# Kernel optimization log

Hardware: AMD Instinct MI355X
Metric: run time of the kernel (lower is better)

Reference implementation:

```python
import jax, jax.numpy as jnp
import numpy as np

NEG_SLOPE = 0.2  # PyG GATConv default leaky_relu slope
N_NODES, IN_DIM, HID, HEADS, OUT = 50000, 128, 64, 4, 128
N_EDGES = 800000


def gat_conv(x, src, dst, num_nodes, W, a_src, a_dst, bias, concat):
    """One PyG-style GATConv (add_self_loops already applied to src/dst)."""
    H, C = a_src.shape
    xp = (x @ W).reshape(num_nodes, H, C)            # (N,H,C)
    s = jnp.einsum('nhc,hc->nh', xp, a_src)          # per-node src score
    d = jnp.einsum('nhc,hc->nh', xp, a_dst)          # per-node dst score
    e = s[src] + d[dst]                              # (E,H)
    e = jnp.where(e > 0, e, NEG_SLOPE * e)           # leaky_relu
    # segment softmax over edges grouped by destination node
    m = jax.ops.segment_max(e, dst, num_segments=num_nodes)
    p = jnp.exp(e - m[dst])
    z = jax.ops.segment_sum(p, dst, num_segments=num_nodes)
    alpha = p / (z[dst] + 1e-16)                     # (E,H)
    # scatter-aggregate messages
    out = jax.ops.segment_sum(xp[src] * alpha[:, :, None], dst, num_segments=num_nodes)
    out = out.reshape(num_nodes, H * C) if concat else out.mean(axis=1)
    return out + bias


def setup_inputs() -> dict:
    key = jax.random.key(0)
    ks = jax.random.split(key, 16)
    HC = HEADS * HID
    inp = {
        'x': jax.random.normal(ks[0], (N_NODES, IN_DIM), dtype=jnp.float32),
        'edge_index': jax.random.randint(ks[1], (2, N_EDGES), 0, N_NODES, dtype=jnp.int32),
        'W0': jax.random.normal(ks[2], (IN_DIM, HC), dtype=jnp.float32) * 0.08,
        'a_src0': jax.random.normal(ks[3], (HEADS, HID), dtype=jnp.float32) * 0.1,
        'a_dst0': jax.random.normal(ks[4], (HEADS, HID), dtype=jnp.float32) * 0.1,
        'b0': jnp.zeros((HC,), dtype=jnp.float32),
        'W1': jax.random.normal(ks[5], (HC, HC), dtype=jnp.float32) * 0.06,
        'a_src1': jax.random.normal(ks[6], (HEADS, HID), dtype=jnp.float32) * 0.1,
        'a_dst1': jax.random.normal(ks[7], (HEADS, HID), dtype=jnp.float32) * 0.1,
        'b1': jnp.zeros((HC,), dtype=jnp.float32),
        'W2': jax.random.normal(ks[8], (HC, OUT), dtype=jnp.float32) * 0.06,
        'a_src2': jax.random.normal(ks[9], (1, OUT), dtype=jnp.float32) * 0.1,
        'a_dst2': jax.random.normal(ks[10], (1, OUT), dtype=jnp.float32) * 0.1,
        'b2': jnp.zeros((OUT,), dtype=jnp.float32),
    }
    return inp


def reference(x, edge_index, W0, a_src0, a_dst0, b0, W1, a_src1, a_dst1, b1, W2, a_src2, a_dst2, b2):
    N = x.shape[0]
    loops = jnp.arange(N, dtype=edge_index.dtype)  # add_self_loops=True
    src = jnp.concatenate([edge_index[0], loops])
    dst = jnp.concatenate([edge_index[1], loops])
    h = gat_conv(x, src, dst, N, W0, a_src0, a_dst0, b0, True)
    h = jax.nn.elu(h)
    h = gat_conv(h, src, dst, N, W1, a_src1, a_dst1, b1, True)
    h = jax.nn.elu(h)
    h = gat_conv(h, src, dst, N, W2, a_src2, a_dst2, b2, False)
    return h
```

## Files before the change

kernel.cpp:

```cpp
#include <hip/hip_runtime.h>
#include <hip/hip_bf16.h>
#include <hip/hip_fp16.h>
#include <math.h>

#define N_NODES 50000
#define N_EDGES 800000
#define ET      (N_EDGES + N_NODES)
#define IN_DIM  128
#define HEADS   4
#define HID     64
#define HC      256
#define OUTD    128

typedef _Float16 half8 __attribute__((ext_vector_type(8)));
typedef float f32x4 __attribute__((ext_vector_type(4)));


__global__ void hist_k(const int* __restrict__ ei, int* __restrict__ counts) {
    int i = blockIdx.x * blockDim.x + threadIdx.x;
    if (i >= ET) return;
    int dv = (i < N_EDGES) ? ei[N_EDGES + i] : (i - N_EDGES);
    atomicAdd(&counts[dv], 1);
}

__global__ void scan1_k(const int* __restrict__ counts, int* __restrict__ offs,
                        int* __restrict__ bsums) {
    __shared__ int sm[512];
    int tid = threadIdx.x;
    int i = blockIdx.x * 512 + tid;
    int v = (i < N_NODES) ? counts[i] : 0;
    sm[tid] = v;
    __syncthreads();
    #pragma unroll
    for (int o = 1; o < 512; o <<= 1) {
        int add = (tid >= o) ? sm[tid - o] : 0;
        __syncthreads();
        sm[tid] += add;
        __syncthreads();
    }
    if (i < N_NODES) offs[i] = sm[tid] - v;
    if (tid == 511) bsums[blockIdx.x] = sm[511];
}

__global__ void scan2_k(int* __restrict__ bsums, int nb) {
    __shared__ int sm[128];
    int tid = threadIdx.x;
    int v = (tid < nb) ? bsums[tid] : 0;
    sm[tid] = v;
    __syncthreads();
    #pragma unroll
    for (int o = 1; o < 128; o <<= 1) {
        int add = (tid >= o) ? sm[tid - o] : 0;
        __syncthreads();
        sm[tid] += add;
        __syncthreads();
    }
    if (tid < nb) bsums[tid] = sm[tid] - v;
}

__global__ void scan3_k(int* __restrict__ offs, const int* __restrict__ bsums) {
    int i = blockIdx.x * 512 + threadIdx.x;
    if (i < N_NODES) offs[i] += bsums[blockIdx.x];
    if (i == 0) offs[N_NODES] = ET;
}

__global__ void fill_k(const int* __restrict__ ei, const int* __restrict__ offs,
                       int* __restrict__ counts, int* __restrict__ csr) {
    int i = blockIdx.x * blockDim.x + threadIdx.x;
    if (i >= ET) return;
    int sv, dv;
    if (i < N_EDGES) { sv = ei[i]; dv = ei[N_EDGES + i]; }
    else             { sv = dv = i - N_EDGES; }
    int pos = offs[dv] + atomicSub(&counts[dv], 1) - 1;
    csr[pos] = sv;
}


__global__ void cvt_fp16_k(const float* __restrict__ x, __half* __restrict__ xh, int n4) {
    int i = blockIdx.x * 256 + threadIdx.x;
    if (i >= n4) return;
    float4 v = *(const float4*)(x + (size_t)i * 4);
    union { __half2 h2[2]; float2 f2; } u;
    u.h2[0] = __floats2half2_rn(v.x, v.y);
    u.h2[1] = __floats2half2_rn(v.z, v.w);
    *(float2*)(xh + (size_t)i * 4) = u.f2;
}

__global__ void prep_k(const float* __restrict__ W0, __half* __restrict__ Wt0,
                       const float* __restrict__ W1, __half* __restrict__ Wt1,
                       const float* __restrict__ W2, __half* __restrict__ Wt2,
                       float* __restrict__ S2, float* __restrict__ D2) {
    int idx = blockIdx.x * 256 + threadIdx.x;
    if (idx < 32768) {
        int n = idx / IN_DIM, k = idx - n * IN_DIM;
        Wt0[idx] = __float2half(W0[(size_t)k * HC + n]);
    } else if (idx < 98304) {
        int i = idx - 32768;
        int n = i / HC, k = i - n * HC;
        Wt1[i] = __float2half(W1[(size_t)k * HC + n]);
    } else if (idx < 131072) {
        int i = idx - 98304;
        int n = i / HC, k = i - n * HC;
        Wt2[i] = __float2half(W2[(size_t)k * OUTD + n]);
    } else if (idx < 181072) {
        S2[idx - 131072] = 0.f;
    } else if (idx < 231072) {
        D2[idx - 181072] = 0.f;
    }
}


__device__ __forceinline__ void async_copy16(void* lds_base, const void* gaddr) {
    __builtin_amdgcn_global_load_lds(
        (const __attribute__((address_space(1))) unsigned int*)gaddr,
        (__attribute__((address_space(3))) unsigned int*)lds_base,
        16, 0, 0);
}

template<int H, int CD, bool ATOMIC>
__global__ __launch_bounds__(256) void gemm_mfma_k(const __half* __restrict__ A,
                                                   const __half* __restrict__ Wt,
                                                   __half* __restrict__ C,
                                                   const float* __restrict__ asrc,
                                                   const float* __restrict__ adst,
                                                   float* __restrict__ S,
                                                   float* __restrict__ D,
                                                   int M, int K, int N) {
    __shared__ __attribute__((aligned(16))) __half Ah[128 * 64];
    __shared__ __attribute__((aligned(16))) __half Bh[128 * 64];
    const int t = threadIdx.x;
    const int w = t >> 6;
    const int lane = t & 63;
    const int wm = w >> 1, wn = w & 1;
    const int row0 = blockIdx.x * 128;
    const int col0 = blockIdx.y * 128;

    f32x4 acc[4][4];
    #pragma unroll
    for (int i = 0; i < 4; ++i)
        #pragma unroll
        for (int j = 0; j < 4; ++j) acc[i][j] = (f32x4){0.f, 0.f, 0.f, 0.f};

    const int srow = lane >> 3;
    const int skq  = (lane & 7) * 8;
    const int fr = lane & 15;
    const int fq = (lane >> 4) * 8;

    for (int k0 = 0; k0 < K; k0 += 64) {
        __syncthreads();
        #pragma unroll
        for (int hh = 0; hh < 4; ++hh) {
            int ra = row0 + w * 32 + hh * 8 + srow;
            if (ra > M - 1) ra = M - 1;
            async_copy16(&Ah[(w * 32 + hh * 8) * 64],
                         A + (size_t)ra * K + k0 + skq);
            int rb = col0 + w * 32 + hh * 8 + srow;
            async_copy16(&Bh[(w * 32 + hh * 8) * 64],
                         Wt + (size_t)rb * K + k0 + skq);
        }
        __syncthreads();
        #pragma unroll
        for (int c = 0; c < 2; ++c) {
            half8 a[4], b[4];
            #pragma unroll
            for (int i = 0; i < 4; ++i)
                a[i] = *(const half8*)&Ah[(wm * 64 + i * 16 + fr) * 64 + c * 32 + fq];
            #pragma unroll
            for (int j = 0; j < 4; ++j)
                b[j] = *(const half8*)&Bh[(wn * 64 + j * 16 + fr) * 64 + c * 32 + fq];
            #pragma unroll
            for (int i = 0; i < 4; ++i)
                #pragma unroll
                for (int j = 0; j < 4; ++j)
                    acc[i][j] = __builtin_amdgcn_mfma_f32_16x16x32_f16(a[i], b[j], acc[i][j], 0, 0, 0);
        }
    }

    const int cr = (lane >> 4) * 4;
    const int cc = lane & 15;
    #pragma unroll
    for (int i = 0; i < 4; ++i) {
        #pragma unroll
        for (int j = 0; j < 4; ++j) {
            int c = col0 + wn * 64 + j * 16 + cc;
            #pragma unroll
            for (int reg = 0; reg < 4; ++reg) {
                int r = row0 + wm * 64 + i * 16 + cr + reg;
                if (r < M)
                    C[(size_t)r * N + c] = __float2half(acc[i][j][reg]);
            }
        }
    }

    const int hh_ = ATOMIC ? 0 : (blockIdx.y * 2 + wn);
    float asj[4], adj[4];
    #pragma unroll
    for (int j = 0; j < 4; ++j) {
        int cwh = (ATOMIC ? wn * 64 : 0) + j * 16 + cc;
        asj[j] = asrc[hh_ * CD + cwh];
        adj[j] = adst[hh_ * CD + cwh];
    }
    #pragma unroll
    for (int i = 0; i < 4; ++i) {
        #pragma unroll
        for (int reg = 0; reg < 4; ++reg) {
            float sv = 0.f, dv = 0.f;
            #pragma unroll
            for (int j = 0; j < 4; ++j) {
                sv = fmaf(acc[i][j][reg], asj[j], sv);
                dv = fmaf(acc[i][j][reg], adj[j], dv);
            }
            #pragma unroll
            for (int o = 1; o < 16; o <<= 1) {
                sv += __shfl_xor(sv, o, 64);
                dv += __shfl_xor(dv, o, 64);
            }
            int r = row0 + wm * 64 + i * 16 + cr + reg;
            if (cc == 0 && r < M) {
                if constexpr (ATOMIC) {
                    atomicAdd(&S[r], sv);
                    atomicAdd(&D[r], dv);
                } else {
                    S[(size_t)r * H + hh_] = sv;
                    D[(size_t)r * H + hh_] = dv;
                }
            }
        }
    }
}


template<int H, int C, bool ELU_OUT, typename OT>
__global__ __launch_bounds__(256) void aggr_k(const __half* __restrict__ xp,
                                              const float* __restrict__ s,
                                              const float* __restrict__ d,
                                              const int* __restrict__ offs,
                                              const int* __restrict__ csr,
                                              const float* __restrict__ bias,
                                              OT* __restrict__ out) {
    constexpr int HCl = H * C;
    constexpr int EPL = HCl / 64;
    constexpr int U = 8;
    int wid = blockIdx.x * 4 + (threadIdx.x >> 6);
    int lane = threadIdx.x & 63;
    if (wid >= N_NODES) return;
    int h = (lane * EPL) / C;
    float dh = d[(size_t)wid * H + h];
    float z = 0.f;
    float acc[EPL];
    #pragma unroll
    for (int k = 0; k < EPL; ++k) acc[k] = 0.f;

    auto loadrow = [&](int src, float* v) {
        const __half* xr = xp + (size_t)src * HCl + lane * EPL;
        if constexpr (EPL == 4) {
            union { float2 f2; __half2 h2[2]; } u;
            u.f2 = *(const float2*)xr;
            float2 a = __half22float2(u.h2[0]);
            float2 b = __half22float2(u.h2[1]);
            v[0] = a.x; v[1] = a.y; v[2] = b.x; v[3] = b.y;
        } else {
            union { float f; __half2 h2; } u;
            u.f = *(const float*)xr;
            float2 a = __half22float2(u.h2);
            v[0] = a.x; v[1] = a.y;
        }
    };

    int e0 = offs[wid], e1 = offs[wid + 1];
    int j = e0;
    for (; j + U <= e1; j += U) {
        int srcs[U];
        #pragma unroll
        for (int u = 0; u < U; ++u) srcs[u] = csr[j + u];
        float ev[U];
        #pragma unroll
        for (int u = 0; u < U; ++u) ev[u] = s[(size_t)srcs[u] * H + h];
        float v[U][EPL];
        #pragma unroll
        for (int u = 0; u < U; ++u) loadrow(srcs[u], v[u]);
        #pragma unroll
        for (int u = 0; u < U; ++u) {
            float e = ev[u] + dh;
            e = (e > 0.f) ? e : 0.2f * e;
            float p = __expf(e);
            z += p;
            #pragma unroll
            for (int k = 0; k < EPL; ++k) acc[k] += p * v[u][k];
        }
    }
    for (; j < e1; ++j) {
        int sv = csr[j];
        float e = s[(size_t)sv * H + h] + dh;
        e = (e > 0.f) ? e : 0.2f * e;
        float p = __expf(e);
        float v[EPL];
        loadrow(sv, v);
        z += p;
        #pragma unroll
        for (int k = 0; k < EPL; ++k) acc[k] += p * v[k];
    }

    float inv = 1.f / (z + 1e-16f);
    float o[EPL];
    #pragma unroll
    for (int k = 0; k < EPL; ++k) {
        o[k] = acc[k] * inv + bias[lane * EPL + k];
        if constexpr (ELU_OUT) o[k] = (o[k] > 0.f) ? o[k] : (__expf(o[k]) - 1.f);
    }
    if constexpr (sizeof(OT) == 2 && EPL == 4) {
        union { __half2 h2[2]; float2 f2; } u;
        u.h2[0] = __floats2half2_rn(o[0], o[1]);
        u.h2[1] = __floats2half2_rn(o[2], o[3]);
        *(float2*)((__half*)out + (size_t)wid * HCl + lane * EPL) = u.f2;
    } else {
        #pragma unroll
        for (int k = 0; k < EPL; ++k)
            out[(size_t)wid * HCl + lane * EPL + k] = (OT)o[k];
    }
}


extern "C" void kernel_launch(void* const* d_in, const int* in_sizes, int n_in,
                              void* d_out, int out_size, void* d_ws, size_t ws_size,
                              hipStream_t stream) {
    const float* x      = (const float*)d_in[0];
    const int*   ei     = (const int*)  d_in[1];
    const float* W0     = (const float*)d_in[2];
    const float* as0    = (const float*)d_in[3];
    const float* ad0    = (const float*)d_in[4];
    const float* b0     = (const float*)d_in[5];
    const float* W1     = (const float*)d_in[6];
    const float* as1    = (const float*)d_in[7];
    const float* ad1    = (const float*)d_in[8];
    const float* b1     = (const float*)d_in[9];
    const float* W2     = (const float*)d_in[10];
    const float* as2    = (const float*)d_in[11];
    const float* ad2    = (const float*)d_in[12];
    const float* b2     = (const float*)d_in[13];
    float* out = (float*)d_out;

    char* p = (char*)d_ws;
    auto take = [&](size_t bytes) {
        char* r = p;
        p += (bytes + 255) & ~(size_t)255;
        return r;
    };
    __half* XPh   = (__half*)take((size_t)N_NODES * HC * 2);
    __half* Hbuf  = (__half*)take((size_t)N_NODES * HC * 2);
    __half* xh    = (__half*)take((size_t)N_NODES * IN_DIM * 2);
    __half* Wt0   = (__half*)take((size_t)IN_DIM * HC * 2);
    __half* Wt1   = (__half*)take((size_t)HC * HC * 2);
    __half* Wt2   = (__half*)take((size_t)HC * OUTD * 2);
    float*  S     = (float*) take((size_t)N_NODES * HEADS * 4);
    float*  D     = (float*) take((size_t)N_NODES * HEADS * 4);
    float*  S2    = (float*) take((size_t)N_NODES * 4);
    float*  D2    = (float*) take((size_t)N_NODES * 4);
    int*    counts= (int*)   take((size_t)N_NODES * 4);
    int*    offs  = (int*)   take((size_t)(N_NODES + 1) * 4);
    int*    bsums = (int*)   take(512 * 4);
    int*    csr   = (int*)   take((size_t)ET * 4);

    const int NB_SCAN = (N_NODES + 511) / 512;
    const int ET_BLOCKS = (ET + 255) / 256;
    const int NODE_BLOCKS = (N_NODES + 3) / 4;

    hipMemsetAsync(counts, 0, (size_t)N_NODES * 4, stream);
    hist_k<<<ET_BLOCKS, 256, 0, stream>>>(ei, counts);
    scan1_k<<<NB_SCAN, 512, 0, stream>>>(counts, offs, bsums);
    scan2_k<<<1, 128, 0, stream>>>(bsums, NB_SCAN);
    scan3_k<<<NB_SCAN, 512, 0, stream>>>(offs, bsums);
    fill_k<<<ET_BLOCKS, 256, 0, stream>>>(ei, offs, counts, csr);

    cvt_fp16_k<<<(N_NODES * IN_DIM / 4 + 255) / 256, 256, 0, stream>>>(x, xh, N_NODES * IN_DIM / 4);
    prep_k<<<(231072 + 255) / 256, 256, 0, stream>>>(W0, Wt0, W1, Wt1, W2, Wt2, S2, D2);

    const int MB = (N_NODES + 127) / 128;
    dim3 g0(MB, HC / 128);
    dim3 g2(MB, OUTD / 128);

    gemm_mfma_k<HEADS, HID, false><<<g0, 256, 0, stream>>>(xh, Wt0, XPh, as0, ad0, S, D, N_NODES, IN_DIM, HC);
    aggr_k<HEADS, HID, true, __half><<<NODE_BLOCKS, 256, 0, stream>>>(XPh, S, D, offs, csr, b0, Hbuf);

    gemm_mfma_k<HEADS, HID, false><<<g0, 256, 0, stream>>>(Hbuf, Wt1, XPh, as1, ad1, S, D, N_NODES, HC, HC);
    aggr_k<HEADS, HID, true, __half><<<NODE_BLOCKS, 256, 0, stream>>>(XPh, S, D, offs, csr, b1, Hbuf);

    gemm_mfma_k<1, OUTD, true><<<g2, 256, 0, stream>>>(Hbuf, Wt2, XPh, as2, ad2, S2, D2, N_NODES, HC, OUTD);
    aggr_k<1, OUTD, false, float><<<NODE_BLOCKS, 256, 0, stream>>>(XPh, S2, D2, offs, csr, b2, out);
}
```

Before: 429.2 us.

## Stage GEMM output through LDS for coalesced stores and merge setup kernels

```diff
diff --git a/kernel.cpp b/kernel.cpp
--- a/kernel.cpp
+++ b/kernel.cpp
@@ -15,13 +15,6 @@
 typedef _Float16 half8 __attribute__((ext_vector_type(8)));
 typedef float f32x4 __attribute__((ext_vector_type(4)));
 
-
-__global__ void hist_k(const int* __restrict__ ei, int* __restrict__ counts) {
-    int i = blockIdx.x * blockDim.x + threadIdx.x;
-    if (i >= ET) return;
-    int dv = (i < N_EDGES) ? ei[N_EDGES + i] : (i - N_EDGES);
-    atomicAdd(&counts[dv], 1);
-}
 
 __global__ void scan1_k(const int* __restrict__ counts, int* __restrict__ offs,
                         int* __restrict__ bsums) {
@@ -76,37 +69,52 @@
 }
 
 
-__global__ void cvt_fp16_k(const float* __restrict__ x, __half* __restrict__ xh, int n4) {
-    int i = blockIdx.x * 256 + threadIdx.x;
-    if (i >= n4) return;
-    float4 v = *(const float4*)(x + (size_t)i * 4);
-    union { __half2 h2[2]; float2 f2; } u;
-    u.h2[0] = __floats2half2_rn(v.x, v.y);
-    u.h2[1] = __floats2half2_rn(v.z, v.w);
-    *(float2*)(xh + (size_t)i * 4) = u.f2;
-}
-
-__global__ void prep_k(const float* __restrict__ W0, __half* __restrict__ Wt0,
-                       const float* __restrict__ W1, __half* __restrict__ Wt1,
-                       const float* __restrict__ W2, __half* __restrict__ Wt2,
-                       float* __restrict__ S2, float* __restrict__ D2) {
-    int idx = blockIdx.x * 256 + threadIdx.x;
-    if (idx < 32768) {
-        int n = idx / IN_DIM, k = idx - n * IN_DIM;
-        Wt0[idx] = __float2half(W0[(size_t)k * HC + n]);
-    } else if (idx < 98304) {
-        int i = idx - 32768;
-        int n = i / HC, k = i - n * HC;
-        Wt1[i] = __float2half(W1[(size_t)k * HC + n]);
-    } else if (idx < 131072) {
-        int i = idx - 98304;
-        int n = i / HC, k = i - n * HC;
-        Wt2[i] = __float2half(W2[(size_t)k * OUTD + n]);
-    } else if (idx < 181072) {
-        S2[idx - 131072] = 0.f;
-    } else if (idx < 231072) {
-        D2[idx - 181072] = 0.f;
-    }
+#define J_HIST  ET
+#define J_CVT   (N_NODES * IN_DIM / 4)
+#define J_W     131072
+#define SETUP_TOTAL (J_HIST + J_CVT + J_W + 2 * N_NODES)
+
+__global__ void setup_k(const int* __restrict__ ei, int* __restrict__ counts,
+                        const float* __restrict__ x, __half* __restrict__ xh,
+                        const float* __restrict__ W0, __half* __restrict__ Wt0,
+                        const float* __restrict__ W1, __half* __restrict__ Wt1,
+                        const float* __restrict__ W2, __half* __restrict__ Wt2,
+                        float* __restrict__ S2, float* __restrict__ D2) {
+    int g = blockIdx.x * 256 + threadIdx.x;
+    if (g < J_HIST) {
+        int dv = (g < N_EDGES) ? ei[N_EDGES + g] : (g - N_EDGES);
+        atomicAdd(&counts[dv], 1);
+        return;
+    }
+    g -= J_HIST;
+    if (g < J_CVT) {
+        float4 v = *(const float4*)(x + (size_t)g * 4);
+        union { __half2 h2[2]; float2 f2; } u;
+        u.h2[0] = __floats2half2_rn(v.x, v.y);
+        u.h2[1] = __floats2half2_rn(v.z, v.w);
+        *(float2*)(xh + (size_t)g * 4) = u.f2;
+        return;
+    }
+    g -= J_CVT;
+    if (g < J_W) {
+        if (g < 32768) {
+            int n = g / IN_DIM, k = g - n * IN_DIM;
+            Wt0[g] = __float2half(W0[(size_t)k * HC + n]);
+        } else if (g < 98304) {
+            int i = g - 32768;
+            int n = i / HC, k = i - n * HC;
+            Wt1[i] = __float2half(W1[(size_t)k * HC + n]);
+        } else {
+            int i = g - 98304;
+            int n = i / HC, k = i - n * HC;
+            Wt2[i] = __float2half(W2[(size_t)k * OUTD + n]);
+        }
+        return;
+    }
+    g -= J_W;
+    if (g < N_NODES) { S2[g] = 0.f; return; }
+    g -= N_NODES;
+    if (g < N_NODES) D2[g] = 0.f;
 }
 
 
@@ -116,6 +124,8 @@
         (__attribute__((address_space(3))) unsigned int*)lds_base,
         16, 0, 0);
 }
+
+#define CPAD 132
 
 template<int H, int CD, bool ATOMIC>
 __global__ __launch_bounds__(256) void gemm_mfma_k(const __half* __restrict__ A,
@@ -126,12 +136,15 @@
                                                    float* __restrict__ S,
                                                    float* __restrict__ D,
                                                    int M, int K, int N) {
-    __shared__ __attribute__((aligned(16))) __half Ah[128 * 64];
-    __shared__ __attribute__((aligned(16))) __half Bh[128 * 64];
+    __shared__ __attribute__((aligned(16))) __half smem[128 * CPAD];
+    __half* Ah = smem;
+    __half* Bh = smem + 128 * 64;
     const int t = threadIdx.x;
     const int w = t >> 6;
     const int lane = t & 63;
     const int wm = w >> 1, wn = w & 1;
+    const int cc = lane & 15;
+    const int quad = lane >> 4;
     const int row0 = blockIdx.x * 128;
     const int col0 = blockIdx.y * 128;
 
@@ -143,8 +156,6 @@
 
     const int srow = lane >> 3;
     const int skq  = (lane & 7) * 8;
-    const int fr = lane & 15;
-    const int fq = (lane >> 4) * 8;
 
     for (int k0 = 0; k0 < K; k0 += 64) {
         __syncthreads();
@@ -164,68 +175,72 @@
             half8 a[4], b[4];
             #pragma unroll
             for (int i = 0; i < 4; ++i)
-                a[i] = *(const half8*)&Ah[(wm * 64 + i * 16 + fr) * 64 + c * 32 + fq];
+                a[i] = *(const half8*)&Ah[(wm * 64 + i * 16 + cc) * 64 + c * 32 + quad * 8];
             #pragma unroll
             for (int j = 0; j < 4; ++j)
-                b[j] = *(const half8*)&Bh[(wn * 64 + j * 16 + fr) * 64 + c * 32 + fq];
+                b[j] = *(const half8*)&Bh[(wn * 64 + j * 16 + cc) * 64 + c * 32 + quad * 8];
             #pragma unroll
             for (int i = 0; i < 4; ++i)
                 #pragma unroll
                 for (int j = 0; j < 4; ++j)
-                    acc[i][j] = __builtin_amdgcn_mfma_f32_16x16x32_f16(a[i], b[j], acc[i][j], 0, 0, 0);
-        }
-    }
-
-    const int cr = (lane >> 4) * 4;
-    const int cc = lane & 15;
+                    acc[i][j] = __builtin_amdgcn_mfma_f32_16x16x32_f16(b[j], a[i], acc[i][j], 0, 0, 0);
+        }
+    }
+
+    const int hh_ = ATOMIC ? 0 : (blockIdx.y * 2 + wn);
+    float4 asj[4], adj[4];
+    #pragma unroll
+    for (int j = 0; j < 4; ++j) {
+        int cb = (ATOMIC ? wn * 64 : 0) + j * 16 + quad * 4;
+        asj[j] = *(const float4*)&asrc[hh_ * CD + cb];
+        adj[j] = *(const float4*)&adst[hh_ * CD + cb];
+    }
     #pragma unroll
     for (int i = 0; i < 4; ++i) {
+        float sv = 0.f, dv = 0.f;
         #pragma unroll
         for (int j = 0; j < 4; ++j) {
-            int c = col0 + wn * 64 + j * 16 + cc;
-            #pragma unroll
-            for (int reg = 0; reg < 4; ++reg) {
-                int r = row0 + wm * 64 + i * 16 + cr + reg;
-                if (r < M)
-                    C[(size_t)r * N + c] = __float2half(acc[i][j][reg]);
+            sv = fmaf(acc[i][j][0], asj[j].x, sv); dv = fmaf(acc[i][j][0], adj[j].x, dv);
+            sv = fmaf(acc[i][j][1], asj[j].y, sv); dv = fmaf(acc[i][j][1], adj[j].y, dv);
+            sv = fmaf(acc[i][j][2], asj[j].z, sv); dv = fmaf(acc[i][j][2], adj[j].z, dv);
+            sv = fmaf(acc[i][j][3], asj[j].w, sv); dv = fmaf(acc[i][j][3], adj[j].w, dv);
+        }
+        sv += __shfl_xor(sv, 16, 64); dv += __shfl_xor(dv, 16, 64);
+        sv += __shfl_xor(sv, 32, 64); dv += __shfl_xor(dv, 32, 64);
+        int r = row0 + wm * 64 + i * 16 + cc;
+        if (quad == 0 && r < M) {
+            if constexpr (ATOMIC) {
+                atomicAdd(&S[r], sv);
+                atomicAdd(&D[r], dv);
+            } else {
+                S[(size_t)r * H + hh_] = sv;
+                D[(size_t)r * H + hh_] = dv;
             }
         }
     }
 
-    const int hh_ = ATOMIC ? 0 : (blockIdx.y * 2 + wn);
-    float asj[4], adj[4];
-    #pragma unroll
-    for (int j = 0; j < 4; ++j) {
-        int cwh = (ATOMIC ? wn * 64 : 0) + j * 16 + cc;
-        asj[j] = asrc[hh_ * CD + cwh];
-        adj[j] = adst[hh_ * CD + cwh];
-    }
+    __syncthreads();
     #pragma unroll
     for (int i = 0; i < 4; ++i) {
-        #pragma unroll
-        for (int reg = 0; reg < 4; ++reg) {
-            float sv = 0.f, dv = 0.f;
-            #pragma unroll
-            for (int j = 0; j < 4; ++j) {
-                sv = fmaf(acc[i][j][reg], asj[j], sv);
-                dv = fmaf(acc[i][j][reg], adj[j], dv);
-            }
-            #pragma unroll
-            for (int o = 1; o < 16; o <<= 1) {
-                sv += __shfl_xor(sv, o, 64);
-                dv += __shfl_xor(dv, o, 64);
-            }
-            int r = row0 + wm * 64 + i * 16 + cr + reg;
-            if (cc == 0 && r < M) {
-                if constexpr (ATOMIC) {
-                    atomicAdd(&S[r], sv);
-                    atomicAdd(&D[r], dv);
-                } else {
-                    S[(size_t)r * H + hh_] = sv;
-                    D[(size_t)r * H + hh_] = dv;
-                }
-            }
-        }
+        int tr = wm * 64 + i * 16 + cc;
+        #pragma unroll
+        for (int j = 0; j < 4; ++j) {
+            int tc = wn * 64 + j * 16 + quad * 4;
+            union { __half2 h2[2]; uint2 u2; } pk;
+            pk.h2[0] = __floats2half2_rn(acc[i][j][0], acc[i][j][1]);
+            pk.h2[1] = __floats2half2_rn(acc[i][j][2], acc[i][j][3]);
+            *(uint2*)&smem[tr * CPAD + tc] = pk.u2;
+        }
+    }
+    __syncthreads();
+    #pragma unroll
+    for (int rr = 0; rr < 8; ++rr) {
+        int r = rr * 16 + (t >> 4);
+        int ccol = (t & 15) * 8;
+        uint4 v = *(const uint4*)&smem[r * CPAD + ccol];
+        int gr = row0 + r;
+        if (gr < M)
+            *(uint4*)&C[(size_t)gr * N + col0 + ccol] = v;
     }
 }
 
@@ -366,15 +381,14 @@
     const int NODE_BLOCKS = (N_NODES + 3) / 4;
 
     hipMemsetAsync(counts, 0, (size_t)N_NODES * 4, stream);
-    hist_k<<<ET_BLOCKS, 256, 0, stream>>>(ei, counts);
+    setup_k<<<(SETUP_TOTAL + 255) / 256, 256, 0, stream>>>(
+        ei, counts, x, xh, W0, Wt0, W1, Wt1, W2, Wt2, S2, D2);
+
     scan1_k<<<NB_SCAN, 512, 0, stream>>>(counts, offs, bsums);
     scan2_k<<<1, 128, 0, stream>>>(bsums, NB_SCAN);
     scan3_k<<<NB_SCAN, 512, 0, stream>>>(offs, bsums);
     fill_k<<<ET_BLOCKS, 256, 0, stream>>>(ei, offs, counts, csr);
 
-    cvt_fp16_k<<<(N_NODES * IN_DIM / 4 + 255) / 256, 256, 0, stream>>>(x, xh, N_NODES * IN_DIM / 4);
-    prep_k<<<(231072 + 255) / 256, 256, 0, stream>>>(W0, Wt0, W1, Wt1, W2, Wt2, S2, D2);
-
     const int MB = (N_NODES + 127) / 128;
     dim3 g0(MB, HC / 128);
     dim3 g2(MB, OUTD / 128);
```

Result: faster. 412.9 us (-3.8%).
